# Optimization experiments

Hardware: AMD Instinct MI355X
Metric: run time of the kernel (lower is better)

Reference implementation:

```python
import jax, jax.numpy as jnp
from jax import lax
import numpy as np

WINDOW_SIZE = 11
SIGMA = 1.5
C1 = 0.01 ** 2
C2 = 0.03 ** 2


def _gauss_1d(n=WINDOW_SIZE, sigma=SIGMA):
    # replicates cv2.getGaussianKernel(n, sigma)
    x = np.arange(n, dtype=np.float64) - (n - 1) / 2.0
    g = np.exp(-(x ** 2) / (2.0 * sigma ** 2))
    return (g / g.sum()).astype(np.float32)


def _blur(x, g):
    """Separable 2D Gaussian blur of x [N,1,H,W]; math equals conv with g g^T."""
    p = g.shape[0] // 2
    kh = g.reshape(1, 1, -1, 1).astype(x.dtype)  # [O,I,KH,1]
    kw = g.reshape(1, 1, 1, -1).astype(x.dtype)  # [O,I,1,KW]
    dn = ('NCHW', 'OIHW', 'NCHW')
    x = lax.conv_general_dilated(x, kh, (1, 1), [(p, p), (0, 0)], dimension_numbers=dn)
    x = lax.conv_general_dilated(x, kw, (1, 1), [(0, 0), (p, p)], dimension_numbers=dn)
    return x


def _ssim_loss_2d(a, b):
    """a, b: [N,1,H,W]. Returns 1 - mean(SSIM map) with the module's exact formula."""
    g = jnp.asarray(_gauss_1d())
    mu1 = _blur(a, g)
    mu2 = _blur(b, g)
    mu1_sq = mu1 * mu1
    mu2_sq = mu2 * mu2
    mu1_mu2 = mu1 * mu2
    sigma1_sq = _blur(a * a, g) - mu1_sq
    sigma2_sq = _blur(b * b, g) - mu2_sq
    sigma12 = _blur(a * b, g) - mu1_mu2
    luminance = (2 * mu1_mu2 + C1) / (mu1_sq + mu2_sq + C1)
    contrast = (2 * sigma12 + C2) / (sigma1_sq + sigma2_sq + C2)
    structure = (sigma12 + C2) / (jnp.sqrt(sigma1_sq) * jnp.sqrt(sigma2_sq) + C2)
    ssim = luminance * contrast * structure
    return 1.0 - ssim.mean()


def setup_inputs() -> dict:
    key = jax.random.key(0)
    k1, k2, k3 = jax.random.split(key, 3)
    img1_3d = jax.random.uniform(k1, (4, 1, 16, 512, 512), dtype=jnp.float32)
    img1_2d = jax.random.uniform(k2, (4, 1, 512, 512), dtype=jnp.float32)
    img2 = jax.random.uniform(k3, (4, 1, 16, 512, 512), dtype=jnp.float32)
    return {"img1_3d": img1_3d, "img1_2d": img1_2d, "img2": img2}


def reference(img1_3d, img1_2d, img2):
    B, C, D, H, W = img1_3d.shape  # C == 1 (forced by groups=C with single-out-channel weight)
    # 3D SSIM: kernel depth 1, depth padding 0 -> per-slice 2D blur; fold D into batch.
    a3 = img1_3d.reshape(B * D, 1, H, W)
    b3 = img2.reshape(B * D, 1, H, W)
    loss3d = _ssim_loss_2d(a3, b3)
    # 2D SSIM against depth-averaged img2.
    b2 = jnp.mean(img2, axis=2)  # [B,1,H,W]
    loss2d = _ssim_loss_2d(img1_2d, b2)
    return loss3d + loss2d
```

## Files before the change

### kernel.cpp

```cpp
#include <hip/hip_runtime.h>
#include <cmath>


#define WSZ 11
#define IMG 512
#define SLICE (IMG * IMG)

typedef float f32x2 __attribute__((ext_vector_type(2)));
typedef float f32x4 __attribute__((ext_vector_type(4)));

struct G11 { float w[WSZ]; };

__device__ __forceinline__ void row_barrier()
{
    asm volatile("s_waitcnt lgkmcnt(0)" ::: "memory");
    __builtin_amdgcn_s_barrier();
}

__global__ __launch_bounds__(256, 4)
void ssim_pk_kernel(const float* __restrict__ A3, const float* __restrict__ B3,
                    const float* __restrict__ A2, const float* __restrict__ B2,
                    double* __restrict__ acc, G11 gw)
{
    __shared__ f32x4 A4[4][262];
    __shared__ f32x4 B4[4][262];
    __shared__ f32x2 Z2[4][262];
    __shared__ float bsum[4];

    const int tx = threadIdx.x;
    const int x0 = tx * 2;

    const int unit = blockIdx.x;
    const float* Ap;
    const float* Bp;
    double* accp;
    int y0, BAND;
    if (unit < 1536) {
        int slice = unit / 24;
        int band  = unit - slice * 24;
        Ap = A3 + (long)slice * SLICE;
        Bp = B3 + (long)slice * SLICE;
        accp = acc + 0;
        if (band < 16) { y0 = band * 22;              BAND = 22; }
        else           { y0 = 352 + (band - 16) * 20; BAND = 20; }
    } else {
        int uu = unit - 1536;
        int img  = uu >> 6;
        int band = uu & 63;
        Ap = A2 + (long)img * SLICE;
        Bp = B2 + (long)img * SLICE;
        accp = acc + 1;
        y0 = band * 8;
        BAND = 8;
    }
    const int ITER = BAND >> 1;

    if (tx < 3) {
        f32x4 z4 = {0.f, 0.f, 0.f, 0.f};
        f32x2 z2 = {0.f, 0.f};
        #pragma unroll
        for (int b = 0; b < 4; b++) {
            A4[b][tx] = z4; A4[b][259 + tx] = z4;
            B4[b][tx] = z4; B4[b][259 + tx] = z4;
            Z2[b][tx] = z2; Z2[b][259 + tx] = z2;
        }
    }

    f32x2 ra[12], rb[12];

    float sum = 0.f;
    const f32x2 C1v = {1e-4f, 1e-4f};
    const f32x2 C2v = {9e-4f, 9e-4f};

    #pragma unroll
    for (int t = 0; t < 10; t++) {
        int r = y0 - 5 + t;
        f32x2 a = {0.f, 0.f}, b = {0.f, 0.f};
        if (r >= 0) {
            a = *(const f32x2*)&Ap[(long)r * IMG + x0];
            b = *(const f32x2*)&Bp[(long)r * IMG + x0];
        }
        ra[t] = a; rb[t] = b;
    }
    ra[10] = (f32x2){0.f, 0.f}; rb[10] = (f32x2){0.f, 0.f};
    ra[11] = (f32x2){0.f, 0.f}; rb[11] = (f32x2){0.f, 0.f};

    f32x2 aN0 = {0.f, 0.f}, bN0 = aN0, aN1 = aN0, bN1 = aN0;
    {
        int r0 = y0 + 5, r1 = y0 + 6;
        if (r0 < IMG) { aN0 = *(const f32x2*)&Ap[(long)r0 * IMG + x0];
                        bN0 = *(const f32x2*)&Bp[(long)r0 * IMG + x0]; }
        if (r1 < IMG) { aN1 = *(const f32x2*)&Ap[(long)r1 * IMG + x0];
                        bN1 = *(const f32x2*)&Bp[(long)r1 * IMG + x0]; }
    }

    auto vpass = [&](int base, int buf) {
        f32x2 m1 = {0.f, 0.f}, m2 = m1, xx = m1, yy = m1, zz = m1;
        #pragma unroll
        for (int j = 0; j < 11; j++) {
            const int s = (base + j) % 12;
            const f32x2 g2 = {gw.w[j], gw.w[j]};
            f32x2 a = ra[s], b = rb[s];
            f32x2 ga = g2 * a, gb = g2 * b;
            m1 += ga; m2 += gb;
            xx += ga * a; yy += gb * b; zz += ga * b;
        }
        A4[buf][3 + tx] = __builtin_shufflevector(m1, m2, 0, 1, 2, 3);
        B4[buf][3 + tx] = __builtin_shufflevector(xx, yy, 0, 1, 2, 3);
        Z2[buf][3 + tx] = zz;
    };

    auto hpass = [&](int buf) {
        f32x2 OM1 = {0.f, 0.f}, OM2 = OM1, OXX = OM1, OYY = OM1, OZZ = OM1;
        {
            f32x4 pa = A4[buf][tx], pb = B4[buf][tx];
            f32x2 pz = Z2[buf][tx];
            const f32x2 c = {gw.w[0], 0.f};
            OM1 += c * __builtin_shufflevector(pa, pa, 1, 1);
            OM2 += c * __builtin_shufflevector(pa, pa, 3, 3);
            OXX += c * __builtin_shufflevector(pb, pb, 1, 1);
            OYY += c * __builtin_shufflevector(pb, pb, 3, 3);
            OZZ += c * __builtin_shufflevector(pz, pz, 1, 1);
        }
        #pragma unroll
        for (int jj = 1; jj <= 5; jj++) {
            f32x4 pa = A4[buf][tx + jj], pb = B4[buf][tx + jj];
            f32x2 pz = Z2[buf][tx + jj];
            const f32x2 cA = {gw.w[2 * jj - 1], gw.w[2 * jj - 2]};
            const f32x2 cB = {gw.w[2 * jj],     gw.w[2 * jj - 1]};
            OM1 += cA * __builtin_shufflevector(pa, pa, 0, 0)
                 + cB * __builtin_shufflevector(pa, pa, 1, 1);
            OM2 += cA * __builtin_shufflevector(pa, pa, 2, 2)
                 + cB * __builtin_shufflevector(pa, pa, 3, 3);
            OXX += cA * __builtin_shufflevector(pb, pb, 0, 0)
                 + cB * __builtin_shufflevector(pb, pb, 1, 1);
            OYY += cA * __builtin_shufflevector(pb, pb, 2, 2)
                 + cB * __builtin_shufflevector(pb, pb, 3, 3);
            OZZ += cA * __builtin_shufflevector(pz, pz, 0, 0)
                 + cB * __builtin_shufflevector(pz, pz, 1, 1);
        }
        {
            f32x4 pa = A4[buf][tx + 6], pb = B4[buf][tx + 6];
            f32x2 pz = Z2[buf][tx + 6];
            const f32x2 c = {0.f, gw.w[10]};
            OM1 += c * __builtin_shufflevector(pa, pa, 0, 0);
            OM2 += c * __builtin_shufflevector(pa, pa, 2, 2);
            OXX += c * __builtin_shufflevector(pb, pb, 0, 0);
            OYY += c * __builtin_shufflevector(pb, pb, 2, 2);
            OZZ += c * __builtin_shufflevector(pz, pz, 0, 0);
        }
        f32x2 m1s = OM1 * OM1, m2s = OM2 * OM2, m12 = OM1 * OM2;
        f32x2 s1 = OXX - m1s, s2 = OYY - m2s, s12 = OZZ - m12;
        f32x2 d1 = m1s + m2s + C1v;
        f32x2 d2 = s1 + s2 + C2v;
        f32x2 num = (2.f * m12 + C1v) * (2.f * s12 + C2v) * (s12 + C2v);
        float d3x = __builtin_amdgcn_sqrtf(s1.x) * __builtin_amdgcn_sqrtf(s2.x) + 9e-4f;
        float d3y = __builtin_amdgcn_sqrtf(s1.y) * __builtin_amdgcn_sqrtf(s2.y) + 9e-4f;
        sum += num.x * __builtin_amdgcn_rcpf(d1.x * d2.x * d3x);
        sum += num.y * __builtin_amdgcn_rcpf(d1.y * d2.y * d3y);
    };

    for (int kk = 0; kk < ITER; kk += 6) {
        #pragma unroll
        for (int u = 0; u < 6; u++) {
            const int k = kk + u;
            if (k < ITER) {
                const int s0 = (10 + 2 * u) % 12;
                const int s1 = (11 + 2 * u) % 12;
                ra[s0] = aN0; rb[s0] = bN0;
                ra[s1] = aN1; rb[s1] = bN1;

                {
                    int r0 = y0 + 7 + 2 * k, r1 = r0 + 1;
                    aN0 = (f32x2){0.f, 0.f}; bN0 = aN0; aN1 = aN0; bN1 = aN0;
                    if (k + 1 < ITER) {
                        if (r0 < IMG) { aN0 = *(const f32x2*)&Ap[(long)r0 * IMG + x0];
                                        bN0 = *(const f32x2*)&Bp[(long)r0 * IMG + x0]; }
                        if (r1 < IMG) { aN1 = *(const f32x2*)&Ap[(long)r1 * IMG + x0];
                                        bN1 = *(const f32x2*)&Bp[(long)r1 * IMG + x0]; }
                    }
                }

                const int b0 = (u & 1) * 2;
                vpass(2 * u,     b0);
                vpass(2 * u + 1, b0 + 1);
                row_barrier();
                hpass(b0);
                hpass(b0 + 1);
            }
        }
    }

    for (int off = 32; off > 0; off >>= 1)
        sum += __shfl_down(sum, off, 64);
    if ((tx & 63) == 0) bsum[tx >> 6] = sum;
    __syncthreads();
    if (tx == 0) {
        float tot = bsum[0] + bsum[1] + bsum[2] + bsum[3];
        atomicAdd(accp, (double)tot);
    }
}

__global__ __launch_bounds__(256) void depth_mean4_kernel(
    const float4* __restrict__ img2, float4* __restrict__ b2)
{
    const int per = SLICE / 4;
    int idx = blockIdx.x * 256 + threadIdx.x;
    int b = idx >> 16;
    int p = idx & (per - 1);
    const float4* src = img2 + (long)b * 16 * per + p;
    float sx = 0.f, sy = 0.f, sz = 0.f, sw = 0.f;
    #pragma unroll
    for (int d = 0; d < 16; d++) {
        float4 v = src[(long)d * per];
        sx += v.x; sy += v.y; sz += v.z; sw += v.w;
    }
    float4 o; o.x = sx * 0.0625f; o.y = sy * 0.0625f; o.z = sz * 0.0625f; o.w = sw * 0.0625f;
    b2[idx] = o;
}

__global__ void finalize_kernel(const double* __restrict__ acc, float* __restrict__ out)
{
    double loss3 = 1.0 - acc[0] / (64.0 * (double)SLICE);
    double loss2 = 1.0 - acc[1] / (4.0 * (double)SLICE);
    out[0] = (float)(loss3 + loss2);
}

extern "C" void kernel_launch(void* const* d_in, const int* in_sizes, int n_in,
                              void* d_out, int out_size, void* d_ws, size_t ws_size,
                              hipStream_t stream)
{
    const float* img1_3d = (const float*)d_in[0];
    const float* img1_2d = (const float*)d_in[1];
    const float* img2    = (const float*)d_in[2];
    float* out = (float*)d_out;

    double* acc = (double*)d_ws;
    float*  b2  = (float*)((char*)d_ws + 256);

    G11 gw;
    {
        double g[WSZ], s = 0.0;
        for (int i = 0; i < WSZ; i++) {
            double xx = (double)i - (WSZ - 1) / 2.0;
            g[i] = std::exp(-(xx * xx) / (2.0 * 1.5 * 1.5));
            s += g[i];
        }
        for (int i = 0; i < WSZ; i++) gw.w[i] = (float)(g[i] / s);
    }

    hipMemsetAsync(acc, 0, 2 * sizeof(double), stream);

    depth_mean4_kernel<<<(4 * SLICE / 4) / 256, 256, 0, stream>>>(
        (const float4*)img2, (float4*)b2);

    ssim_pk_kernel<<<1792, 256, 0, stream>>>(img1_3d, img2, img1_2d, b2, acc, gw);

    finalize_kernel<<<1, 1, 0, stream>>>(acc, out);
}
```

Before: 93.98 us.

## Process four rows per iteration with taller 32-row bands and fewer blocks

```diff
diff --git a/kernel.cpp b/kernel.cpp
--- a/kernel.cpp
+++ b/kernel.cpp
@@ -17,7 +17,7 @@
     __builtin_amdgcn_s_barrier();
 }
 
-__global__ __launch_bounds__(256, 4)
+__global__ __launch_bounds__(256, 3)
 void ssim_pk_kernel(const float* __restrict__ A3, const float* __restrict__ B3,
                     const float* __restrict__ A2, const float* __restrict__ B2,
                     double* __restrict__ acc, G11 gw)
@@ -35,16 +35,16 @@
     const float* Bp;
     double* accp;
     int y0, BAND;
-    if (unit < 1536) {
-        int slice = unit / 24;
-        int band  = unit - slice * 24;
+    if (unit < 1024) {
+        int slice = unit >> 4;
+        int band  = unit & 15;
         Ap = A3 + (long)slice * SLICE;
         Bp = B3 + (long)slice * SLICE;
         accp = acc + 0;
-        if (band < 16) { y0 = band * 22;              BAND = 22; }
-        else           { y0 = 352 + (band - 16) * 20; BAND = 20; }
+        y0 = band * 32;
+        BAND = 32;
     } else {
-        int uu = unit - 1536;
+        int uu = unit - 1024;
         int img  = uu >> 6;
         int band = uu & 63;
         Ap = A2 + (long)img * SLICE;
@@ -53,7 +53,7 @@
         y0 = band * 8;
         BAND = 8;
     }
-    const int ITER = BAND >> 1;
+    const int ITER = BAND >> 2;
 
     if (tx < 3) {
         f32x4 z4 = {0.f, 0.f, 0.f, 0.f};
@@ -66,7 +66,7 @@
         }
     }
 
-    f32x2 ra[12], rb[12];
+    f32x2 ra[16], rb[16];
 
     float sum = 0.f;
     const f32x2 C1v = {1e-4f, 1e-4f};
@@ -82,23 +82,28 @@
         }
         ra[t] = a; rb[t] = b;
     }
-    ra[10] = (f32x2){0.f, 0.f}; rb[10] = (f32x2){0.f, 0.f};
-    ra[11] = (f32x2){0.f, 0.f}; rb[11] = (f32x2){0.f, 0.f};
+    #pragma unroll
+    for (int t = 10; t < 16; t++) { ra[t] = (f32x2){0.f, 0.f}; rb[t] = (f32x2){0.f, 0.f}; }
 
     f32x2 aN0 = {0.f, 0.f}, bN0 = aN0, aN1 = aN0, bN1 = aN0;
+    f32x2 aN2 = aN0, bN2 = aN0, aN3 = aN0, bN3 = aN0;
     {
-        int r0 = y0 + 5, r1 = y0 + 6;
-        if (r0 < IMG) { aN0 = *(const f32x2*)&Ap[(long)r0 * IMG + x0];
-                        bN0 = *(const f32x2*)&Bp[(long)r0 * IMG + x0]; }
-        if (r1 < IMG) { aN1 = *(const f32x2*)&Ap[(long)r1 * IMG + x0];
-                        bN1 = *(const f32x2*)&Bp[(long)r1 * IMG + x0]; }
+        int r = y0 + 5;
+        if (r     < IMG) { aN0 = *(const f32x2*)&Ap[(long)(r    ) * IMG + x0];
+                           bN0 = *(const f32x2*)&Bp[(long)(r    ) * IMG + x0]; }
+        if (r + 1 < IMG) { aN1 = *(const f32x2*)&Ap[(long)(r + 1) * IMG + x0];
+                           bN1 = *(const f32x2*)&Bp[(long)(r + 1) * IMG + x0]; }
+        if (r + 2 < IMG) { aN2 = *(const f32x2*)&Ap[(long)(r + 2) * IMG + x0];
+                           bN2 = *(const f32x2*)&Bp[(long)(r + 2) * IMG + x0]; }
+        if (r + 3 < IMG) { aN3 = *(const f32x2*)&Ap[(long)(r + 3) * IMG + x0];
+                           bN3 = *(const f32x2*)&Bp[(long)(r + 3) * IMG + x0]; }
     }
 
     auto vpass = [&](int base, int buf) {
         f32x2 m1 = {0.f, 0.f}, m2 = m1, xx = m1, yy = m1, zz = m1;
         #pragma unroll
         for (int j = 0; j < 11; j++) {
-            const int s = (base + j) % 12;
+            const int s = (base + j) % 16;
             const f32x2 g2 = {gw.w[j], gw.w[j]};
             f32x2 a = ra[s], b = rb[s];
             f32x2 ga = g2 * a, gb = g2 * b;
@@ -160,33 +165,46 @@
         sum += num.y * __builtin_amdgcn_rcpf(d1.y * d2.y * d3y);
     };
 
-    for (int kk = 0; kk < ITER; kk += 6) {
-        #pragma unroll
-        for (int u = 0; u < 6; u++) {
+    for (int kk = 0; kk < ITER; kk += 4) {
+        #pragma unroll
+        for (int u = 0; u < 4; u++) {
             const int k = kk + u;
             if (k < ITER) {
-                const int s0 = (10 + 2 * u) % 12;
-                const int s1 = (11 + 2 * u) % 12;
+                const int s0 = (10 + 4 * u) % 16;
+                const int s1 = (11 + 4 * u) % 16;
+                const int s2 = (12 + 4 * u) % 16;
+                const int s3 = (13 + 4 * u) % 16;
                 ra[s0] = aN0; rb[s0] = bN0;
                 ra[s1] = aN1; rb[s1] = bN1;
+                ra[s2] = aN2; rb[s2] = bN2;
+                ra[s3] = aN3; rb[s3] = bN3;
 
                 {
-                    int r0 = y0 + 7 + 2 * k, r1 = r0 + 1;
+                    int r = y0 + 9 + 4 * k;
                     aN0 = (f32x2){0.f, 0.f}; bN0 = aN0; aN1 = aN0; bN1 = aN0;
+                    aN2 = aN0; bN2 = aN0; aN3 = aN0; bN3 = aN0;
                     if (k + 1 < ITER) {
-                        if (r0 < IMG) { aN0 = *(const f32x2*)&Ap[(long)r0 * IMG + x0];
-                                        bN0 = *(const f32x2*)&Bp[(long)r0 * IMG + x0]; }
-                        if (r1 < IMG) { aN1 = *(const f32x2*)&Ap[(long)r1 * IMG + x0];
-                                        bN1 = *(const f32x2*)&Bp[(long)r1 * IMG + x0]; }
+                        if (r     < IMG) { aN0 = *(const f32x2*)&Ap[(long)(r    ) * IMG + x0];
+                                           bN0 = *(const f32x2*)&Bp[(long)(r    ) * IMG + x0]; }
+                        if (r + 1 < IMG) { aN1 = *(const f32x2*)&Ap[(long)(r + 1) * IMG + x0];
+                                           bN1 = *(const f32x2*)&Bp[(long)(r + 1) * IMG + x0]; }
+                        if (r + 2 < IMG) { aN2 = *(const f32x2*)&Ap[(long)(r + 2) * IMG + x0];
+                                           bN2 = *(const f32x2*)&Bp[(long)(r + 2) * IMG + x0]; }
+                        if (r + 3 < IMG) { aN3 = *(const f32x2*)&Ap[(long)(r + 3) * IMG + x0];
+                                           bN3 = *(const f32x2*)&Bp[(long)(r + 3) * IMG + x0]; }
                     }
                 }
 
-                const int b0 = (u & 1) * 2;
-                vpass(2 * u,     b0);
-                vpass(2 * u + 1, b0 + 1);
+                vpass((4 * u + 0) % 16, 0);
+                vpass((4 * u + 1) % 16, 1);
+                vpass((4 * u + 2) % 16, 2);
+                vpass((4 * u + 3) % 16, 3);
                 row_barrier();
-                hpass(b0);
-                hpass(b0 + 1);
+                hpass(0);
+                hpass(1);
+                hpass(2);
+                hpass(3);
+                row_barrier();
             }
         }
     }
@@ -254,7 +272,7 @@
     depth_mean4_kernel<<<(4 * SLICE / 4) / 256, 256, 0, stream>>>(
         (const float4*)img2, (float4*)b2);
 
-    ssim_pk_kernel<<<1792, 256, 0, stream>>>(img1_3d, img2, img1_2d, b2, acc, gw);
+    ssim_pk_kernel<<<1280, 256, 0, stream>>>(img1_3d, img2, img1_2d, b2, acc, gw);
 
     finalize_kernel<<<1, 1, 0, stream>>>(acc, out);
 }
```

Result: slower. 116.7 us (+24.2%).
